# Performance work log

Hardware: AMD Instinct MI355X
Metric: run time of the kernel (lower is better)

## Reference

```python
import jax, jax.numpy as jnp
import numpy as np


def setup_inputs() -> dict:
    key = jax.random.key(0)
    k0, k1, k2, k3, k4 = jax.random.split(key, 5)
    Ns, N, D = 1024, 192, 24
    # spins in {-1, +1}
    x = (2.0 * jax.random.randint(k0, (Ns, N), 0, 2) - 1.0).astype(jnp.float32)
    # symmetric distance-index matrix with values in [0, D)
    r = jax.random.randint(k1, (N, N), 0, D)
    nd = jnp.minimum(r, r.T).astype(jnp.int32)
    W2 = 0.1 * jax.random.normal(k2, (D,), dtype=jnp.float32)
    W3 = 0.01 * jax.random.normal(k3, (D, D), dtype=jnp.float32)
    # positive mean-field coefficients so log(phi) is real
    phi = 0.5 + jax.random.uniform(k4, (N, 2), dtype=jnp.float32)
    return {"x": x, "W2": W2, "W3": W3, "phi": phi, "neighbors_distances": nd}


def reference(x, W2, W3, phi, neighbors_distances):
    # x: (Ns, N) spins in {-1,+1}; W2: (D,); W3: (D,D); phi: (N,2); nd: (N,N) int in [0,D)
    nd = neighbors_distances
    N = x.shape[-1]

    # J2[n] = 0.5 * sum_{i,j} x[n,i] * W2[nd[i,j]] * x[n,j]
    J2 = 0.5 * jnp.einsum('ni,ij,nj->n', x, W2[nd], x)

    # J3[n] = sum_{i,j,k} W3[nd[k,j], nd[i,j]] x[n,k] x[n,i] x[n,j]
    G = W3[nd]                                  # (N,N,D): G[k,j,d] = W3[nd[k,j], d]
    S = jnp.einsum('nk,kjd->njd', x, G)         # (Ns,N,D)
    j_idx = jnp.broadcast_to(jnp.arange(N)[None, :], (N, N))
    M = S[:, j_idx, nd]                         # (Ns,N,N): M[n,i,j] = S[n, j, nd[i,j]]
    J3 = jnp.einsum('nij,ni,nj->n', M, x, x)

    # mean-field: sum_i log(phi[i, (1+x[n,i])/2])
    idx = jax.lax.stop_gradient(((1.0 + x) * 0.5)).astype(jnp.int32)  # (Ns,N) in {0,1}
    mf = phi[jnp.arange(N)[None, :], idx]       # (Ns,N)
    logmf = jnp.sum(jnp.log(mf), axis=-1)

    return J2 + J3 + logmf
```

## Files before the change

### kernel.cpp

```cpp
#include <hip/hip_runtime.h>
#include <math.h>


#define NS 1024
#define NN 192
#define DD 24

typedef unsigned long long ull;

#define M_WORDS (NN * DD * 8)

__global__ __launch_bounds__(192) void prep_kernel(
    const float* __restrict__ x,
    const float* __restrict__ phi,
    const int*   __restrict__ nd,
    unsigned* __restrict__ Mbuf,
    unsigned* __restrict__ Pd,
    float* __restrict__ out)
{
    const int tid = threadIdx.x;
    const int wv  = tid >> 6;
    const int b   = blockIdx.x;

    if (b < NN) {
        const int j   = b;
        const int ndv = nd[j * NN + tid];
        #pragma unroll
        for (int r = 0; r < DD; ++r) {
            ull m = __ballot(ndv == r);
            if ((tid & 63) == 0) {
                unsigned* dst = &Mbuf[(j * DD + r) * 8 + 2 * wv];
                dst[0] = (unsigned)m;
                dst[1] = (unsigned)(m >> 32);
            }
        }
    } else {
        const int n   = b - NN;
        const float xv = x[n * NN + tid];
        const int bit  = (xv > 0.0f) ? 1 : 0;
        ull m = __ballot(bit);
        if ((tid & 63) == 0) {
            Pd[(2 * wv    ) * NS + n] = (unsigned)m;
            Pd[(2 * wv + 1) * NS + n] = (unsigned)(m >> 32);
        }
        float contrib = logf(phi[tid * 2 + bit]);
        __shared__ float red[3];
        #pragma unroll
        for (int off = 32; off >= 1; off >>= 1)
            contrib += __shfl_down(contrib, off, 64);
        if ((tid & 63) == 0) red[wv] = contrib;
        __syncthreads();
        if (tid == 0) out[n] = red[0] + red[1] + red[2];
    }
}

__global__ __launch_bounds__(256) void main_kernel(
    const float* __restrict__ W2,
    const float* __restrict__ W3,
    const unsigned* __restrict__ Mbuf,
    const unsigned* __restrict__ Pd,
    float* __restrict__ out)
{
    const int lane = threadIdx.x & 63;
    const int wv   = threadIdx.x >> 6;
    const int n    = blockIdx.x * 64 + lane;
    int j = blockIdx.y * 4 + wv;
    j = __builtin_amdgcn_readfirstlane(j);

    const unsigned p0 = Pd[0 * NS + n];
    const unsigned p1 = Pd[1 * NS + n];
    const unsigned p2 = Pd[2 * NS + n];
    const unsigned p3 = Pd[3 * NS + n];
    const unsigned p4 = Pd[4 * NS + n];
    const unsigned p5 = Pd[5 * NS + n];

    const unsigned* __restrict__ Mj = &Mbuf[j * DD * 8];

    float c[DD];
    #pragma unroll
    for (int r = 0; r < DD; ++r) {
        const unsigned m0 = Mj[r * 8 + 0];
        const unsigned m1 = Mj[r * 8 + 1];
        const unsigned m2 = Mj[r * 8 + 2];
        const unsigned m3 = Mj[r * 8 + 3];
        const unsigned m4 = Mj[r * 8 + 4];
        const unsigned m5 = Mj[r * 8 + 5];
        int pc = __popc(m0 & p0) + __popc(m1 & p1) + __popc(m2 & p2)
               + __popc(m3 & p3) + __popc(m4 & p4) + __popc(m5 & p5);
        int cnt = __popcll(((ull)m1 << 32) | m0)
                + __popcll(((ull)m3 << 32) | m2)
                + __popcll(((ull)m5 << 32) | m4);
        c[r] = fmaf(2.0f, (float)pc, -(float)cnt);
    }

    float q = 0.0f, l2 = 0.0f;
    #pragma unroll
    for (int r = 0; r < DD; ++r) {
        float t = 0.0f;
        #pragma unroll
        for (int s = 0; s < DD; ++s) t = fmaf(W3[r * DD + s], c[s], t);
        q  = fmaf(c[r], t, q);
        l2 = fmaf(W2[r], c[r], l2);
    }

    const int w = j >> 5, bpos = j & 31;
    unsigned pw = (w == 0) ? p0 : (w == 1) ? p1 : (w == 2) ? p2
                : (w == 3) ? p3 : (w == 4) ? p4 : p5;
    const float xj = ((pw >> bpos) & 1u) ? 1.0f : -1.0f;

    const float contrib = xj * fmaf(0.5f, l2, q);
    unsafeAtomicAdd(&out[n], contrib);
}

extern "C" void kernel_launch(void* const* d_in, const int* in_sizes, int n_in,
                              void* d_out, int out_size, void* d_ws, size_t ws_size,
                              hipStream_t stream) {
    const float* x   = (const float*)d_in[0];
    const float* W2  = (const float*)d_in[1];
    const float* W3  = (const float*)d_in[2];
    const float* phi = (const float*)d_in[3];
    const int*   nd  = (const int*)d_in[4];
    float* out = (float*)d_out;

    unsigned* Mbuf = (unsigned*)d_ws;
    unsigned* Pd   = (unsigned*)d_ws + M_WORDS;

    prep_kernel<<<NN + NS, 192, 0, stream>>>(x, phi, nd, Mbuf, Pd, out);
    main_kernel<<<dim3(NS / 64, NN / 4), 256, 0, stream>>>(W2, W3, Mbuf, Pd, out);
}
```

Measured before the change: 28.07 us.

## Symmetrize W3 quadratic form, precompute mask counts, reduce atomics per block

Prep now folds W3 into an upper-triangular symmetric matrix Q, so the quadratic form c^T W3 c in the main kernel uses about half as many FMAs. It also stores the negated per-row mask count as a float in the Mbuf padding slot, which removes the repeated popcounts in the main kernel. The main kernel grows to 512 threads with 8 j-values per block, and partial sums are reduced in shared memory so each block issues one atomic per sample instead of one per wave. The costs are an extra prep block, a block-wide barrier, and summation order that differs from the original.

```diff
diff --git a/kernel.cpp b/kernel.cpp
--- a/kernel.cpp
+++ b/kernel.cpp
@@ -9,13 +9,16 @@
 typedef unsigned long long ull;
 
 #define M_WORDS (NN * DD * 8)
+#define P_WORDS (6 * NS)
 
 __global__ __launch_bounds__(192) void prep_kernel(
     const float* __restrict__ x,
+    const float* __restrict__ W3,
     const float* __restrict__ phi,
     const int*   __restrict__ nd,
     unsigned* __restrict__ Mbuf,
     unsigned* __restrict__ Pd,
+    float* __restrict__ Qbuf,
     float* __restrict__ out)
 {
     const int tid = threadIdx.x;
@@ -25,17 +28,30 @@
     if (b < NN) {
         const int j   = b;
         const int ndv = nd[j * NN + tid];
+        __shared__ unsigned smask[DD][6];
         #pragma unroll
         for (int r = 0; r < DD; ++r) {
             ull m = __ballot(ndv == r);
             if ((tid & 63) == 0) {
-                unsigned* dst = &Mbuf[(j * DD + r) * 8 + 2 * wv];
-                dst[0] = (unsigned)m;
-                dst[1] = (unsigned)(m >> 32);
+                smask[r][2 * wv]     = (unsigned)m;
+                smask[r][2 * wv + 1] = (unsigned)(m >> 32);
             }
         }
-    } else {
-        const int n   = b - NN;
+        __syncthreads();
+        const int r = tid >> 3, w = tid & 7;
+        unsigned v;
+        if (w < 6) {
+            v = smask[r][w];
+        } else if (w == 6) {
+            int cnt = __popc(smask[r][0]) + __popc(smask[r][1]) + __popc(smask[r][2])
+                    + __popc(smask[r][3]) + __popc(smask[r][4]) + __popc(smask[r][5]);
+            v = __float_as_uint(-(float)cnt);
+        } else {
+            v = 0u;
+        }
+        Mbuf[(j * DD + r) * 8 + w] = v;
+    } else if (b < NN + NS) {
+        const int n    = b - NN;
         const float xv = x[n * NN + tid];
         const int bit  = (xv > 0.0f) ? 1 : 0;
         ull m = __ballot(bit);
@@ -51,12 +67,20 @@
         if ((tid & 63) == 0) red[wv] = contrib;
         __syncthreads();
         if (tid == 0) out[n] = red[0] + red[1] + red[2];
+    } else {
+        for (int t = tid; t < DD * DD; t += 192) {
+            const int r = t / DD, s = t % DD;
+            float q = 0.0f;
+            if (s > r)       q = W3[r * DD + s] + W3[s * DD + r];
+            else if (s == r) q = W3[r * DD + r];
+            Qbuf[t] = q;
+        }
     }
 }
 
-__global__ __launch_bounds__(256) void main_kernel(
+__global__ __launch_bounds__(512) void main_kernel(
     const float* __restrict__ W2,
-    const float* __restrict__ W3,
+    const float* __restrict__ Qbuf,
     const unsigned* __restrict__ Mbuf,
     const unsigned* __restrict__ Pd,
     float* __restrict__ out)
@@ -64,7 +88,7 @@
     const int lane = threadIdx.x & 63;
     const int wv   = threadIdx.x >> 6;
     const int n    = blockIdx.x * 64 + lane;
-    int j = blockIdx.y * 4 + wv;
+    int j = blockIdx.y * 8 + wv;
     j = __builtin_amdgcn_readfirstlane(j);
 
     const unsigned p0 = Pd[0 * NS + n];
@@ -85,20 +109,18 @@
         const unsigned m3 = Mj[r * 8 + 3];
         const unsigned m4 = Mj[r * 8 + 4];
         const unsigned m5 = Mj[r * 8 + 5];
+        const float ncnt  = __uint_as_float(Mj[r * 8 + 6]);
         int pc = __popc(m0 & p0) + __popc(m1 & p1) + __popc(m2 & p2)
                + __popc(m3 & p3) + __popc(m4 & p4) + __popc(m5 & p5);
-        int cnt = __popcll(((ull)m1 << 32) | m0)
-                + __popcll(((ull)m3 << 32) | m2)
-                + __popcll(((ull)m5 << 32) | m4);
-        c[r] = fmaf(2.0f, (float)pc, -(float)cnt);
+        c[r] = fmaf(2.0f, (float)pc, ncnt);
     }
 
     float q = 0.0f, l2 = 0.0f;
     #pragma unroll
     for (int r = 0; r < DD; ++r) {
-        float t = 0.0f;
+        float t = Qbuf[r * DD + r] * c[r];
         #pragma unroll
-        for (int s = 0; s < DD; ++s) t = fmaf(W3[r * DD + s], c[s], t);
+        for (int s = r + 1; s < DD; ++s) t = fmaf(Qbuf[r * DD + s], c[s], t);
         q  = fmaf(c[r], t, q);
         l2 = fmaf(W2[r], c[r], l2);
     }
@@ -108,8 +130,16 @@
                 : (w == 3) ? p3 : (w == 4) ? p4 : p5;
     const float xj = ((pw >> bpos) & 1u) ? 1.0f : -1.0f;
 
-    const float contrib = xj * fmaf(0.5f, l2, q);
-    unsafeAtomicAdd(&out[n], contrib);
+    const float acc = xj * fmaf(0.5f, l2, q);
+
+    __shared__ float part[8][64];
+    part[wv][lane] = acc;
+    __syncthreads();
+    if (wv == 0) {
+        float s = part[0][lane] + part[1][lane] + part[2][lane] + part[3][lane]
+                + part[4][lane] + part[5][lane] + part[6][lane] + part[7][lane];
+        unsafeAtomicAdd(&out[n], s);
+    }
 }
 
 extern "C" void kernel_launch(void* const* d_in, const int* in_sizes, int n_in,
@@ -123,8 +153,9 @@
     float* out = (float*)d_out;
 
     unsigned* Mbuf = (unsigned*)d_ws;
-    unsigned* Pd   = (unsigned*)d_ws + M_WORDS;
+    unsigned* Pd   = Mbuf + M_WORDS;
+    float*    Qbuf = (float*)(Pd + P_WORDS);
 
-    prep_kernel<<<NN + NS, 192, 0, stream>>>(x, phi, nd, Mbuf, Pd, out);
-    main_kernel<<<dim3(NS / 64, NN / 4), 256, 0, stream>>>(W2, W3, Mbuf, Pd, out);
+    prep_kernel<<<NN + NS + 1, 192, 0, stream>>>(x, W3, phi, nd, Mbuf, Pd, Qbuf, out);
+    main_kernel<<<dim3(NS / 64, NN / 8), 512, 0, stream>>>(W2, Qbuf, Mbuf, Pd, out);
 }
```

Measured after the change: 30.15 us. 1.07x slower.
